# Kernel optimization log

Hardware: AMD Instinct MI355X
Metric: run time of the kernel (lower is better)

## Reference

```python
import jax, jax.numpy as jnp
import numpy as np

B, S, D, H = 4, 1024, 1024, 16
DH = D // H
RD = float(np.sqrt(D))


def linear_vdp(mu_a, var_a, mu_b, var_b):
    # Product of two independent random matrices: E[AB], Var[AB] (elementwise)
    mean = mu_a @ mu_b
    var = var_a @ var_b + var_a @ (mu_b ** 2) + (mu_a ** 2) @ var_b
    return mean, var


def softmax_vdp(a, var_a):
    # p = softmax(a); variance via squared Jacobian J_ij = p_i(delta_ij - p_j):
    # var_out_i = p_i^2 * (sum_j p_j^2 var_j + var_i * (1 - 2 p_i))
    p = jax.nn.softmax(a, axis=-1)
    s = jnp.sum(p * p * var_a, axis=-1, keepdims=True)
    var_out = p * p * (s + var_a * (1.0 - 2.0 * p))
    return p, var_out


def setup_inputs() -> dict:
    key = jax.random.key(0)
    ks = jax.random.split(key, 8)
    x = jax.random.normal(ks[0], (B, S, D), dtype=jnp.float32)
    var_x = jax.random.uniform(ks[1], (B, S, D), dtype=jnp.float32) * 0.1
    k = jax.random.normal(ks[2], (B, H, S, DH), dtype=jnp.float32)
    var_k = jax.random.uniform(ks[3], (B, H, S, DH), dtype=jnp.float32) * 0.1
    v = jax.random.normal(ks[4], (B, H, S, DH), dtype=jnp.float32)
    var_v = jax.random.uniform(ks[5], (B, H, S, DH), dtype=jnp.float32) * 0.1
    # LinearVDP(d, d, bias=False): weight mean + (positive) weight variance
    Wq_mu = jax.random.normal(ks[6], (D, D), dtype=jnp.float32) / np.sqrt(D)
    Wq_var = jax.random.uniform(ks[7], (D, D), dtype=jnp.float32) * (0.1 / D)
    return {"x": x, "var_x": var_x, "k": k, "var_k": var_k, "v": v,
            "var_v": var_v, "Wq_mu": Wq_mu, "Wq_var": Wq_var}


def reference(x, var_x, k, var_k, v, var_v, Wq_mu, Wq_var):
    # LinearVDP projection (y = x W^T with random weight)
    q = x @ Wq_mu.T
    var_q = var_x @ Wq_var.T + var_x @ (Wq_mu ** 2).T + (x ** 2) @ Wq_var.T
    # split heads: [B,S,D] -> [B,H,S,DH]
    q = q.reshape(B, S, H, DH).transpose(0, 2, 1, 3)
    var_q = var_q.reshape(B, S, H, DH).transpose(0, 2, 1, 3)
    # scores with variance propagation
    a, var_a = linear_vdp(q, var_q, jnp.swapaxes(k, 2, 3), jnp.swapaxes(var_k, 2, 3))
    a = a / RD
    var_a = var_a / (RD ** 2)
    # causal mask (-inf above diagonal) on the mean path only
    causal = jnp.triu(jnp.ones((S, S), dtype=bool), k=1)
    a = jnp.where(causal, -jnp.inf, a)
    a, var_a = softmax_vdp(a, var_a)
    # attention * values with variance propagation
    a, var_a = linear_vdp(a, var_a, v, var_v)
    # merge heads: [B,H,S,DH] -> [B,S,D]
    a = a.transpose(0, 2, 1, 3).reshape(B, S, D)
    var_a = var_a.transpose(0, 2, 1, 3).reshape(B, S, D)
    return x + a, var_a
```

## Files before the change

kernel.cpp:

```cpp
#include <hip/hip_runtime.h>
#include <hip/hip_bf16.h>
#include <math.h>

#define NB 4
#define NS 1024
#define ND 1024
#define NH 16
#define NDH 64
#define M4 4194304
#define M1 1048576

typedef float f16v __attribute__((ext_vector_type(16)));
typedef short bf8 __attribute__((ext_vector_type(8)));
typedef unsigned short ushort_t;

union U8 { bf8 v; unsigned u[4]; unsigned short s[8]; };

__device__ __forceinline__ unsigned pk(float lo, float hi) {
    __hip_bfloat162 h2 = __float22bfloat162_rn(make_float2(lo, hi));
    return *reinterpret_cast<unsigned*>(&h2);
}
__device__ __forceinline__ unsigned short f2b(float f) {
    unsigned u = __float_as_uint(f);
    unsigned r = (u + 0x7fffu + ((u >> 16) & 1u)) >> 16;
    return (unsigned short)r;
}
__device__ __forceinline__ float b2f(unsigned short h) {
    return __uint_as_float(((unsigned)h) << 16);
}
__device__ __forceinline__ f16v zero16() {
    f16v z;
    #pragma unroll
    for (int i = 0; i < 16; ++i) z[i] = 0.f;
    return z;
}
__device__ __forceinline__ void vscale(f16v& v, float s) {
    #pragma unroll
    for (int i = 0; i < 16; ++i) v[i] *= s;
}

__device__ __forceinline__ void gl_lds16(const ushort_t* g, ushort_t* l) {
    __builtin_amdgcn_global_load_lds(
        (const __attribute__((address_space(1))) unsigned int*)g,
        (__attribute__((address_space(3))) unsigned int*)l,
        16, 0, 0);
}

__device__ __forceinline__ bf8 mkB(unsigned p0, unsigned p1, unsigned p2, unsigned p3, int h) {
    unsigned own0 = h ? p2 : p0;
    unsigned own1 = h ? p3 : p1;
    unsigned ct0  = h ? p0 : p2;
    unsigned ct1  = h ? p1 : p3;
    unsigned x0 = (unsigned)__shfl_xor((int)ct0, 32);
    unsigned x1 = (unsigned)__shfl_xor((int)ct1, 32);
    U8 B;
    B.u[0] = h ? x0 : own0;
    B.u[1] = h ? x1 : own1;
    B.u[2] = h ? own0 : x0;
    B.u[3] = h ? own1 : x1;
    return B.v;
}


__global__ __launch_bounds__(256)
void prep_all(const float* __restrict__ x, const float* __restrict__ vx,
              const float* __restrict__ K,  const float* __restrict__ VK,
              const float* __restrict__ Vv, const float* __restrict__ VV,
              const float* __restrict__ Wm, const float* __restrict__ Wv,
              ushort_t* __restrict__ kmF, ushort_t* __restrict__ k2F, ushort_t* __restrict__ kvF,
              ushort_t* __restrict__ vmF, ushort_t* __restrict__ wF,  ushort_t* __restrict__ vvF,
              ushort_t* __restrict__ fx, ushort_t* __restrict__ fvx, ushort_t* __restrict__ fx2,
              ushort_t* __restrict__ fm, ushort_t* __restrict__ fw2, ushort_t* __restrict__ fv)
{
    __shared__ ushort_t Lm[2048], Lw[2048], Lv[2048];
    const int tid = threadIdx.x;
    const int bid = blockIdx.x;

    if (bid < 2048) {
        const int bh = bid >> 5, s = bid & 31;
        const int jp  = tid >> 3;
        const int dh0 = (tid & 7) * 8;
        const size_t gin = ((size_t)bh * NS + s * 32 + jp) * NDH + dh0;
        const size_t sbase = ((size_t)bh * 32 + s) * 2048;

        float kk[8], uu[8], vm[8], vv[8];
        *(float4*)(kk)   = *(const float4*)(K  + gin); *(float4*)(kk+4) = *(const float4*)(K  + gin + 4);
        *(float4*)(uu)   = *(const float4*)(VK + gin); *(float4*)(uu+4) = *(const float4*)(VK + gin + 4);
        *(float4*)(vm)   = *(const float4*)(Vv + gin); *(float4*)(vm+4) = *(const float4*)(Vv + gin + 4);
        *(float4*)(vv)   = *(const float4*)(VV + gin); *(float4*)(vv+4) = *(const float4*)(VV + gin + 4);

        const size_t kout = sbase + (size_t)((tid & 7) >> 1) * 512
                          + (jp + 32 * ((tid & 7) & 1)) * 8;
        unsigned o0[4], o1[4], o2[4];
        #pragma unroll
        for (int t = 0; t < 4; ++t) {
            o0[t] = pk(kk[2*t], kk[2*t+1]);
            o1[t] = pk(fmaf(kk[2*t],kk[2*t],uu[2*t]), fmaf(kk[2*t+1],kk[2*t+1],uu[2*t+1]));
            o2[t] = pk(uu[2*t], uu[2*t+1]);
        }
        *(uint4*)(kmF + kout) = make_uint4(o0[0],o0[1],o0[2],o0[3]);
        *(uint4*)(k2F + kout) = make_uint4(o1[0],o1[1],o1[2],o1[3]);
        *(uint4*)(kvF + kout) = make_uint4(o2[0],o2[1],o2[2],o2[3]);

        #pragma unroll
        for (int e = 0; e < 8; ++e) {
            const int dh = dh0 + e;
            const int idx = ((dh >> 5) * 2 + (jp >> 4)) * 512
                          + ((dh & 31) + 32 * ((jp >> 3) & 1)) * 8 + (jp & 7);
            Lm[idx] = f2b(vm[e]);
            Lw[idx] = f2b(fmaf(vm[e], vm[e], vv[e]));
            Lv[idx] = f2b(vv[e]);
        }
        __syncthreads();
        const size_t vout = sbase + (size_t)tid * 8;
        *(uint4*)(vmF + vout) = *(const uint4*)(Lm + tid * 8);
        *(uint4*)(wF  + vout) = *(const uint4*)(Lw + tid * 8);
        *(uint4*)(vvF + vout) = *(const uint4*)(Lv + tid * 8);
    } else {
        const size_t g = (size_t)(bid - 2048) * 256 + tid;
        if (g < 524288) {
            const size_t g0 = g * 8;
            const int row = (int)(g0 >> 10), k0 = (int)(g0 & 1023);
            const size_t fo = ((size_t)(row >> 5) * 64 + (k0 >> 4)) * 512
                            + ((row & 31) + 32 * ((k0 >> 3) & 1)) * 8;
            float a[8], c[8];
            *(float4*)(a)   = *(const float4*)(x + g0);  *(float4*)(a+4) = *(const float4*)(x + g0 + 4);
            *(float4*)(c)   = *(const float4*)(vx + g0); *(float4*)(c+4) = *(const float4*)(vx + g0 + 4);
            *(uint4*)(fx  + fo) = make_uint4(pk(a[0],a[1]), pk(a[2],a[3]), pk(a[4],a[5]), pk(a[6],a[7]));
            *(uint4*)(fvx + fo) = make_uint4(pk(c[0],c[1]), pk(c[2],c[3]), pk(c[4],c[5]), pk(c[6],c[7]));
            *(uint4*)(fx2 + fo) = make_uint4(pk(a[0]*a[0],a[1]*a[1]), pk(a[2]*a[2],a[3]*a[3]),
                                             pk(a[4]*a[4],a[5]*a[5]), pk(a[6]*a[6],a[7]*a[7]));
        } else {
            const size_t g0 = (g - 524288) * 8;
            const int row = (int)(g0 >> 10), k0 = (int)(g0 & 1023);
            const size_t fo = ((size_t)(row >> 5) * 64 + (k0 >> 4)) * 512
                            + ((row & 31) + 32 * ((k0 >> 3) & 1)) * 8;
            float a[8], c[8];
            *(float4*)(a)   = *(const float4*)(Wm + g0); *(float4*)(a+4) = *(const float4*)(Wm + g0 + 4);
            *(float4*)(c)   = *(const float4*)(Wv + g0); *(float4*)(c+4) = *(const float4*)(Wv + g0 + 4);
            *(uint4*)(fm  + fo) = make_uint4(pk(a[0],a[1]), pk(a[2],a[3]), pk(a[4],a[5]), pk(a[6],a[7]));
            *(uint4*)(fv  + fo) = make_uint4(pk(c[0],c[1]), pk(c[2],c[3]), pk(c[4],c[5]), pk(c[6],c[7]));
            *(uint4*)(fw2 + fo) = make_uint4(pk(fmaf(a[0],a[0],c[0]), fmaf(a[1],a[1],c[1])),
                                             pk(fmaf(a[2],a[2],c[2]), fmaf(a[3],a[3],c[3])),
                                             pk(fmaf(a[4],a[4],c[4]), fmaf(a[5],a[5],c[5])),
                                             pk(fmaf(a[6],a[6],c[6]), fmaf(a[7],a[7],c[7])));
        }
    }
}

__global__ __launch_bounds__(256, 2)
void qproj_b(const ushort_t* __restrict__ xplanes,
             const ushort_t* __restrict__ wplanes,
             ushort_t* __restrict__ qmF, ushort_t* __restrict__ vqF)
{
    __shared__ ushort_t wstg[3][12 * 512];

    const int tid  = threadIdx.x;
    const int w    = tid >> 6;
    const int lane = tid & 63;
    const int lh   = lane & 31;
    const int h    = lane >> 5;
    const int blk  = blockIdx.x;
    const int lb   = (blk & 7) * 64 + (blk >> 3);
    const int mb   = (lb >> 6) * 4 + ((lb & 63) >> 4);
    const int head = lb & 15;
    const int mt   = mb * 4 + w;
    const int nt   = head * 2 + (w & 1);

    f16v aQ0 = zero16(), aQ1 = zero16(), aV0 = zero16(), aV1 = zero16();

    const ushort_t* xb = xplanes + (size_t)mt * 64 * 512 + lane * 8;
    const ushort_t* wsrc = wplanes + ((size_t)nt * 64 + (w >> 1)) * 512 + lane * 8;

    #pragma unroll
    for (int q = 0; q < 3; ++q)
        gl_lds16(wsrc + (size_t)q * M1, &wstg[0][(3 * w + q) * 512 + lane * 8]);
    #pragma unroll
    for (int q = 0; q < 3; ++q)
        gl_lds16(wsrc + (size_t)q * M1 + 2 * 512, &wstg[1][(3 * w + q) * 512 + lane * 8]);

    bf8 xc[6], xn[6];
    #pragma unroll
    for (int kcL = 0; kcL < 2; ++kcL)
        #pragma unroll
        for (int q = 0; q < 3; ++q)
            xc[3 * kcL + q] = *(const bf8*)(xb + (size_t)q * M4 + kcL * 512);

    for (int t = 0; t < 32; ++t) {
        const int cur = t % 3;
        if (t < 31) asm volatile("s_waitcnt vmcnt(9)" ::: "memory");
        else        asm volatile("s_waitcnt vmcnt(6)" ::: "memory");
        __builtin_amdgcn_s_barrier();
        if (t + 2 < 32) {
            const int nxt = (t + 2) % 3;
            #pragma unroll
            for (int q = 0; q < 3; ++q)
                gl_lds16(wsrc + (size_t)q * M1 + (size_t)(2 * (t + 2)) * 512,
                         &wstg[nxt][(3 * w + q) * 512 + lane * 8]);
        }
        __builtin_amdgcn_sched_barrier(0);
        if (t + 1 < 32) {
            #pragma unroll
            for (int kcL = 0; kcL < 2; ++kcL)
                #pragma unroll
                for (int q = 0; q < 3; ++q)
                    xn[3 * kcL + q] = *(const bf8*)(xb + (size_t)q * M4 + (2 * (t + 1) + kcL) * 512);
        }
        const ushort_t* sc = wstg[cur];
        __builtin_amdgcn_s_setprio(1);
        #pragma unroll
        for (int kcL = 0; kcL < 2; ++kcL) {
            bf8 bx  = xc[3 * kcL + 0];
            bf8 bvx = xc[3 * kcL + 1];
            bf8 bx2 = xc[3 * kcL + 2];
            bf8 A0m = *(const bf8*)(sc + (3 * (2 * kcL + 0) + 0) * 512 + lane * 8);
            bf8 A0w = *(const bf8*)(sc + (3 * (2 * kcL + 0) + 1) * 512 + lane * 8);
            bf8 A0v = *(const bf8*)(sc + (3 * (2 * kcL + 0) + 2) * 512 + lane * 8);
            bf8 A1m = *(const bf8*)(sc + (3 * (2 * kcL + 1) + 0) * 512 + lane * 8);
            bf8 A1w = *(const bf8*)(sc + (3 * (2 * kcL + 1) + 1) * 512 + lane * 8);
            bf8 A1v = *(const bf8*)(sc + (3 * (2 * kcL + 1) + 2) * 512 + lane * 8);
            aQ0 = __builtin_amdgcn_mfma_f32_32x32x16_bf16(A0m, bx,  aQ0, 0, 0, 0);
            aV0 = __builtin_amdgcn_mfma_f32_32x32x16_bf16(A0w, bvx, aV0, 0, 0, 0);
            aV0 = __builtin_amdgcn_mfma_f32_32x32x16_bf16(A0v, bx2, aV0, 0, 0, 0);
            aQ1 = __builtin_amdgcn_mfma_f32_32x32x16_bf16(A1m, bx,  aQ1, 0, 0, 0);
            aV1 = __builtin_amdgcn_mfma_f32_32x32x16_bf16(A1w, bvx, aV1, 0, 0, 0);
            aV1 = __builtin_amdgcn_mfma_f32_32x32x16_bf16(A1v, bx2, aV1, 0, 0, 0);
        }
        __builtin_amdgcn_s_setprio(0);
        asm volatile("s_waitcnt lgkmcnt(0)" ::: "memory");
        __builtin_amdgcn_sched_barrier(0);
        #pragma unroll
        for (int q = 0; q < 6; ++q) xc[q] = xn[q];
    }

    const int mrow = mt * 32 + lh;
    const int b = mrow >> 10;
    const int rt = mt & 31;
    const size_t bh_base = ((size_t)(b * NH + head)) * 65536 + (size_t)rt * 2048;
    const float S1 = 0.03125f, S2 = 0.0009765625f;
    #pragma unroll
    for (int i = 0; i < 16; i += 2) {
        const int dh0 = (i & 3) + 8 * (i >> 2) + 4 * h;
        const size_t o = bh_base + (size_t)(dh0 >> 4) * 512
                       + (lh + 32 * ((dh0 >> 3) & 1)) * 8 + (dh0 & 7);
        *(unsigned*)(qmF + o)         = pk(aQ0[i]*S1, aQ0[i+1]*S1);
        *(unsigned*)(qmF + o + 1024)  = pk(aQ1[i]*S1, aQ1[i+1]*S1);
        *(unsigned*)(vqF + o)         = pk(aV0[i]*S2, aV0[i+1]*S2);
        *(unsigned*)(vqF + o + 1024)  = pk(aV1[i]*S2, aV1[i+1]*S2);
    }
}

__global__ __launch_bounds__(256, 2)
void attn_b(const ushort_t* __restrict__ qmF, const ushort_t* __restrict__ vqF,
            const ushort_t* __restrict__ planes,
            const float* __restrict__ x,
            float* __restrict__ out0, float* __restrict__ out1)
{
    __shared__ union {
        ushort_t stg[3][6 * 2048];
        float ep[128][66];
    } sm;

    const int tid  = threadIdx.x;
    const int w    = tid >> 6;
    const int lane = tid & 63;
    const int lh   = lane & 31;
    const int h    = lane >> 5;
    const int blk  = blockIdx.x;
    const int lb   = (blk & 7) * 64 + (blk >> 3);
    const int rb   = 7 - (lb & 7);
    const int bh   = lb >> 3;
    const int rt   = rb * 4 + w;
    const size_t base = (size_t)bh * 65536;

    bf8 fqm[4], fvq[4], fq2[4];
    {
        const ushort_t* qp = qmF + base + (size_t)rt * 2048 + lane * 8;
        const ushort_t* vp = vqF + base + (size_t)rt * 2048 + lane * 8;
        #pragma unroll
        for (int c = 0; c < 4; ++c) {
            fqm[c] = *(const bf8*)(qp + c * 512);
            fvq[c] = *(const bf8*)(vp + c * 512);
            U8 t; t.v = fqm[c];
            U8 r;
            #pragma unroll
            for (int k = 0; k < 4; ++k) {
                float q0 = b2f(t.s[2*k]), q1 = b2f(t.s[2*k+1]);
                r.u[k] = pk(q0*q0, q1*q1);
            }
            fq2[c] = r.v;
        }
    }

    f16v aN1[2], aN2w[2], aM2[2], aN3[2];
    #pragma unroll
    for (int dt = 0; dt < 2; ++dt) { aN1[dt]=zero16(); aN2w[dt]=zero16(); aM2[dt]=zero16(); aN3[dt]=zero16(); }
    float mrun = -INFINITY, Zrun = 0.f, S2run = 0.f;

    const int nstage = 4 * rb + 4;
    #pragma unroll
    for (int p = 0; p < 6; ++p)
        gl_lds16(planes + (size_t)p * M4 + base + w * 512 + lane * 8,
                 &sm.stg[0][p * 2048 + w * 512 + lane * 8]);
    #pragma unroll
    for (int p = 0; p < 6; ++p)
        gl_lds16(planes + (size_t)p * M4 + base + 2048 + w * 512 + lane * 8,
                 &sm.stg[1][p * 2048 + w * 512 + lane * 8]);

    for (int st = 0; st < nstage; ++st) {
        const int cur = st % 3;
        if (st + 2 < nstage) {
            const int nxt = (st + 2) % 3;
            #pragma unroll
            for (int p = 0; p < 6; ++p)
                gl_lds16(planes + (size_t)p * M4 + base + (size_t)(st + 2) * 2048 + w * 512 + lane * 8,
                         &sm.stg[nxt][p * 2048 + w * 512 + lane * 8]);
            asm volatile("s_waitcnt vmcnt(12)" ::: "memory");
        } else if (st + 1 < nstage) {
            asm volatile("s_waitcnt vmcnt(6)" ::: "memory");
        } else {
            asm volatile("s_waitcnt vmcnt(0)" ::: "memory");
        }
        __builtin_amdgcn_s_barrier();
        __builtin_amdgcn_sched_barrier(0);

        if (st <= rt) {
            __builtin_amdgcn_s_setprio(1);
            const ushort_t* sb = sm.stg[cur];
            f16v accA = zero16(), accU = zero16();
            #pragma unroll
            for (int c = 0; c < 4; ++c) {
                bf8 A0 = *(const bf8*)(sb + 0 * 2048 + c * 512 + lane * 8);
                bf8 A1 = *(const bf8*)(sb + 1 * 2048 + c * 512 + lane * 8);
                bf8 A2 = *(const bf8*)(sb + 2 * 2048 + c * 512 + lane * 8);
                accA = __builtin_amdgcn_mfma_f32_32x32x16_bf16(A0, fqm[c], accA, 0, 0, 0);
                accU = __builtin_amdgcn_mfma_f32_32x32x16_bf16(A1, fvq[c], accU, 0, 0, 0);
                accU = __builtin_amdgcn_mfma_f32_32x32x16_bf16(A2, fq2[c], accU, 0, 0, 0);
            }
            if (st == rt) {
                #pragma unroll
                for (int i = 0; i < 16; ++i) {
                    const int jl = (i & 3) + 8 * (i >> 2) + 4 * h;
                    if (jl > lh) accA[i] = -INFINITY;
                }
            }
            float t8[8];
            #pragma unroll
            for (int i = 0; i < 8; ++i) t8[i] = fmaxf(accA[i], accA[i + 8]);
            #pragma unroll
            for (int i = 0; i < 4; ++i) t8[i] = fmaxf(t8[i], t8[i + 4]);
            float mx = fmaxf(fmaxf(t8[0], t8[1]), fmaxf(t8[2], t8[3]));
            mx = fmaxf(mx, __shfl_xor(mx, 32));
            if (!__all(mx <= mrun + 8.f)) {
                const float mnew = fmaxf(mrun, mx);
                const float s1 = __expf(mrun - mnew);
                const float s2 = s1 * s1, s3 = s2 * s1;
                Zrun *= s1; S2run *= s2;
                #pragma unroll
                for (int dt = 0; dt < 2; ++dt) { vscale(aN1[dt],s1); vscale(aN2w[dt],s2); vscale(aM2[dt],s2); vscale(aN3[dt],s3); }
                mrun = mnew;
            }
            float zt[8], sq[8];
            #pragma unroll
            for (int i = 0; i < 16; ++i) accA[i] = __expf(accA[i] - mrun);
            #pragma unroll
            for (int i = 0; i < 8; ++i) {
                zt[i] = accA[i] + accA[i + 8];
                sq[i] = fmaf(accA[i] * accA[i], accU[i],
                             accA[i + 8] * accA[i + 8] * accU[i + 8]);
            }
            #pragma unroll
            for (int i = 0; i < 4; ++i) { zt[i] += zt[i + 4]; sq[i] += sq[i + 4]; }
            float Zt = (zt[0] + zt[1]) + (zt[2] + zt[3]);
            float St = (sq[0] + sq[1]) + (sq[2] + sq[3]);
            Zt += __shfl_xor(Zt, 32); St += __shfl_xor(St, 32);
            Zrun += Zt; S2run += St;

            #pragma unroll
            for (int c2 = 0; c2 < 2; ++c2) {
                unsigned pE[4], pE2[4], pEU[4], pE3[4];
                #pragma unroll
                for (int k = 0; k < 4; ++k) {
                    const int i0 = 8*c2 + 2*k;
                    const float e0 = accA[i0], e1 = accA[i0+1];
                    const float q0 = e0*e0, q1 = e1*e1;
                    const float t0 = q0*accU[i0], t1 = q1*accU[i0+1];
                    pE [k] = pk(e0, e1);
                    pE2[k] = pk(q0, q1);
                    pEU[k] = pk(t0, t1);
                    pE3[k] = pk(t0*e0, t1*e1);
                }
                bf8 BE  = mkB(pE [0], pE [1], pE [2], pE [3], h);
                bf8 BE2 = mkB(pE2[0], pE2[1], pE2[2], pE2[3], h);
                bf8 BEU = mkB(pEU[0], pEU[1], pEU[2], pEU[3], h);
                bf8 BE3 = mkB(pE3[0], pE3[1], pE3[2], pE3[3], h);
                #pragma unroll
                for (int dt = 0; dt < 2; ++dt) {
                    const ushort_t* vp = sb + 3 * 2048 + (dt * 2 + c2) * 512 + lane * 8;
                    bf8 Am = *(const bf8*)(vp + 0 * 2048);
                    bf8 Aw = *(const bf8*)(vp + 1 * 2048);
                    bf8 Av = *(const bf8*)(vp + 2 * 2048);
                    aN1[dt]  = __builtin_amdgcn_mfma_f32_32x32x16_bf16(Am, BE,  aN1[dt],  0, 0, 0);
                    aN2w[dt] = __builtin_amdgcn_mfma_f32_32x32x16_bf16(Aw, BE2, aN2w[dt], 0, 0, 0);
                    aM2[dt]  = __builtin_amdgcn_mfma_f32_32x32x16_bf16(Aw, BEU, aM2[dt],  0, 0, 0);
                    aM2[dt]  = __builtin_amdgcn_mfma_f32_32x32x16_bf16(Av, BE2, aM2[dt],  0, 0, 0);
                    aN3[dt]  = __builtin_amdgcn_mfma_f32_32x32x16_bf16(Aw, BE3, aN3[dt],  0, 0, 0);
                }
            }
            __builtin_amdgcn_s_setprio(0);
        }
        __builtin_amdgcn_sched_barrier(0);
        __builtin_amdgcn_s_barrier();
    }

    const float rZ  = 1.f / Zrun;
    const float rZ2 = rZ * rZ;
    const float sS  = S2run * rZ2;
    const int b = bh >> 4, head = bh & 15;

    #pragma unroll
    for (int dt = 0; dt < 2; ++dt)
        #pragma unroll
        for (int i = 0; i < 16; ++i) {
            const int col = 32*dt + (i & 3) + 8*(i >> 2) + 4*h;
            sm.ep[w*32 + lh][col] = aN1[dt][i] * rZ;
        }
    __syncthreads();
    {
        const int row = tid >> 1, half = (tid & 1) * 32;
        const size_t o = ((size_t)b * NS + rb*128 + row) * ND + head * NDH + half;
        #pragma unroll
        for (int q4 = 0; q4 < 32; q4 += 4) {
            float4 t = make_float4(sm.ep[row][half+q4], sm.ep[row][half+q4+1],
                                   sm.ep[row][half+q4+2], sm.ep[row][half+q4+3]);
            float4 xi = *(const float4*)(x + o + q4);
            *(float4*)(out0 + o + q4) = make_float4(t.x+xi.x, t.y+xi.y, t.z+xi.z, t.w+xi.w);
        }
    }
    __syncthreads();
    #pragma unroll
    for (int dt = 0; dt < 2; ++dt)
        #pragma unroll
        for (int i = 0; i < 16; ++i) {
            const int col = 32*dt + (i & 3) + 8*(i >> 2) + 4*h;
            sm.ep[w*32 + lh][col] = rZ2 * fmaf(sS, aN2w[dt][i], aM2[dt][i]) - 2.f*rZ2*rZ*aN3[dt][i];
        }
    __syncthreads();
    {
        const int row = tid >> 1, half = (tid & 1) * 32;
        const size_t o = ((size_t)b * NS + rb*128 + row) * ND + head * NDH + half;
        #pragma unroll
        for (int q4 = 0; q4 < 32; q4 += 4) {
            float4 t = make_float4(sm.ep[row][half+q4], sm.ep[row][half+q4+1],
                                   sm.ep[row][half+q4+2], sm.ep[row][half+q4+3]);
            *(float4*)(out1 + o + q4) = t;
        }
    }
}

extern "C" void kernel_launch(void* const* d_in, const int* in_sizes, int n_in,
                              void* d_out, int out_size, void* d_ws, size_t ws_size,
                              hipStream_t stream)
{
    (void)in_sizes; (void)n_in; (void)out_size; (void)ws_size;
    const float* x  = (const float*)d_in[0];
    const float* vx = (const float*)d_in[1];
    const float* K  = (const float*)d_in[2];
    const float* VK = (const float*)d_in[3];
    const float* Vv = (const float*)d_in[4];
    const float* VV = (const float*)d_in[5];
    const float* Wm = (const float*)d_in[6];
    const float* Wv = (const float*)d_in[7];

    float* out0 = (float*)d_out;
    float* out1 = out0 + (size_t)NB * NS * ND;

    ushort_t* qm  = (ushort_t*)d_ws;
    ushort_t* vq  = qm  + M4;
    ushort_t* kmF = vq  + M4;
    ushort_t* k2F = kmF + M4;
    ushort_t* kvF = k2F + M4;
    ushort_t* vmF = kvF + M4;
    ushort_t* wF  = vmF + M4;
    ushort_t* vvF = wF  + M4;
    ushort_t* fxF = vvF + M4;
    ushort_t* fvxF= fxF + M4;
    ushort_t* fx2F= fvxF+ M4;
    ushort_t* fmF = fx2F+ M4;
    ushort_t* fw2F= fmF + M1;
    ushort_t* fvF = fw2F+ M1;

    prep_all<<<4608, 256, 0, stream>>>(x, vx, K, VK, Vv, VV, Wm, Wv,
                                       kmF, k2F, kvF, vmF, wF, vvF,
                                       fxF, fvxF, fx2F, fmF, fw2F, fvF);
    qproj_b<<<512, 256, 0, stream>>>(fxF, fmF, qm, vq);
    attn_b<<<512, 256, 0, stream>>>(qm, vq, kmF, x, out0, out1);
}
```

Before: 167.9 us.

## Fuse Q projection into attention kernel, keeping Q fragments in registers

Merges the Q/var_q projection kernel into the attention kernel. Each block computes its own 128-row by head tile of q and var_q, packs the accumulators straight into MFMA operand fragments with mkB, and then runs attention. This drops the workspace round trip for qm/vq and one kernel launch. In exchange, the block-to-tile mapping changes so projection and attention tiles line up, which gives up the previous causal load-balancing order and may raise register pressure.

```diff
diff --git a/kernel.cpp b/kernel.cpp
--- a/kernel.cpp
+++ b/kernel.cpp
@@ -149,11 +149,17 @@
 }
 
 __global__ __launch_bounds__(256, 2)
-void qproj_b(const ushort_t* __restrict__ xplanes,
-             const ushort_t* __restrict__ wplanes,
-             ushort_t* __restrict__ qmF, ushort_t* __restrict__ vqF)
+void attn_fused(const ushort_t* __restrict__ xplanes,
+                const ushort_t* __restrict__ wplanes,
+                const ushort_t* __restrict__ planes,
+                const float* __restrict__ x,
+                float* __restrict__ out0, float* __restrict__ out1)
 {
-    __shared__ ushort_t wstg[3][12 * 512];
+    __shared__ union {
+        ushort_t wstg[3][12 * 512];
+        ushort_t stg[3][6 * 2048];
+        float ep[128][66];
+    } sm;
 
     const int tid  = threadIdx.x;
     const int w    = tid >> 6;
@@ -162,10 +168,17 @@
     const int h    = lane >> 5;
     const int blk  = blockIdx.x;
     const int lb   = (blk & 7) * 64 + (blk >> 3);
-    const int mb   = (lb >> 6) * 4 + ((lb & 63) >> 4);
+    const int xcd  = lb >> 6;
     const int head = lb & 15;
-    const int mt   = mb * 4 + w;
-    const int nt   = head * 2 + (w & 1);
+    const int g    = (lb >> 4) & 3;
+    const int b    = g;
+    const int rb   = (2 * g + xcd) & 7;
+    const int bh   = b * 16 + head;
+    const int rt   = rb * 4 + w;
+    const size_t base = (size_t)bh * 65536;
+
+    const int mt = b * 32 + rb * 4 + w;
+    const int nt = head * 2 + (w & 1);
 
     f16v aQ0 = zero16(), aQ1 = zero16(), aV0 = zero16(), aV1 = zero16();
 
@@ -174,10 +187,10 @@
 
     #pragma unroll
     for (int q = 0; q < 3; ++q)
-        gl_lds16(wsrc + (size_t)q * M1, &wstg[0][(3 * w + q) * 512 + lane * 8]);
+        gl_lds16(wsrc + (size_t)q * M1, &sm.wstg[0][(3 * w + q) * 512 + lane * 8]);
     #pragma unroll
     for (int q = 0; q < 3; ++q)
-        gl_lds16(wsrc + (size_t)q * M1 + 2 * 512, &wstg[1][(3 * w + q) * 512 + lane * 8]);
+        gl_lds16(wsrc + (size_t)q * M1 + 2 * 512, &sm.wstg[1][(3 * w + q) * 512 + lane * 8]);
 
     bf8 xc[6], xn[6];
     #pragma unroll
@@ -196,7 +209,7 @@
             #pragma unroll
             for (int q = 0; q < 3; ++q)
                 gl_lds16(wsrc + (size_t)q * M1 + (size_t)(2 * (t + 2)) * 512,
-                         &wstg[nxt][(3 * w + q) * 512 + lane * 8]);
+                         &sm.wstg[nxt][(3 * w + q) * 512 + lane * 8]);
         }
         __builtin_amdgcn_sched_barrier(0);
         if (t + 1 < 32) {
@@ -206,7 +219,7 @@
                 for (int q = 0; q < 3; ++q)
                     xn[3 * kcL + q] = *(const bf8*)(xb + (size_t)q * M4 + (2 * (t + 1) + kcL) * 512);
         }
-        const ushort_t* sc = wstg[cur];
+        const ushort_t* sc = sm.wstg[cur];
         __builtin_amdgcn_s_setprio(1);
         #pragma unroll
         for (int kcL = 0; kcL < 2; ++kcL) {
@@ -233,54 +246,21 @@
         for (int q = 0; q < 6; ++q) xc[q] = xn[q];
     }
 
-    const int mrow = mt * 32 + lh;
-    const int b = mrow >> 10;
-    const int rt = mt & 31;
-    const size_t bh_base = ((size_t)(b * NH + head)) * 65536 + (size_t)rt * 2048;
-    const float S1 = 0.03125f, S2 = 0.0009765625f;
-    #pragma unroll
-    for (int i = 0; i < 16; i += 2) {
-        const int dh0 = (i & 3) + 8 * (i >> 2) + 4 * h;
-        const size_t o = bh_base + (size_t)(dh0 >> 4) * 512
-                       + (lh + 32 * ((dh0 >> 3) & 1)) * 8 + (dh0 & 7);
-        *(unsigned*)(qmF + o)         = pk(aQ0[i]*S1, aQ0[i+1]*S1);
-        *(unsigned*)(qmF + o + 1024)  = pk(aQ1[i]*S1, aQ1[i+1]*S1);
-        *(unsigned*)(vqF + o)         = pk(aV0[i]*S2, aV0[i+1]*S2);
-        *(unsigned*)(vqF + o + 1024)  = pk(aV1[i]*S2, aV1[i+1]*S2);
-    }
-}
-
-__global__ __launch_bounds__(256, 2)
-void attn_b(const ushort_t* __restrict__ qmF, const ushort_t* __restrict__ vqF,
-            const ushort_t* __restrict__ planes,
-            const float* __restrict__ x,
-            float* __restrict__ out0, float* __restrict__ out1)
-{
-    __shared__ union {
-        ushort_t stg[3][6 * 2048];
-        float ep[128][66];
-    } sm;
-
-    const int tid  = threadIdx.x;
-    const int w    = tid >> 6;
-    const int lane = tid & 63;
-    const int lh   = lane & 31;
-    const int h    = lane >> 5;
-    const int blk  = blockIdx.x;
-    const int lb   = (blk & 7) * 64 + (blk >> 3);
-    const int rb   = 7 - (lb & 7);
-    const int bh   = lb >> 3;
-    const int rt   = rb * 4 + w;
-    const size_t base = (size_t)bh * 65536;
-
     bf8 fqm[4], fvq[4], fq2[4];
     {
-        const ushort_t* qp = qmF + base + (size_t)rt * 2048 + lane * 8;
-        const ushort_t* vp = vqF + base + (size_t)rt * 2048 + lane * 8;
+        const float S1 = 0.03125f, S2 = 0.0009765625f;
+        unsigned Uq[16], Uv[16];
+        #pragma unroll
+        for (int k = 0; k < 8; ++k) {
+            Uq[k]     = pk(aQ0[2*k] * S1, aQ0[2*k+1] * S1);
+            Uq[8 + k] = pk(aQ1[2*k] * S1, aQ1[2*k+1] * S1);
+            Uv[k]     = pk(aV0[2*k] * S2, aV0[2*k+1] * S2);
+            Uv[8 + k] = pk(aV1[2*k] * S2, aV1[2*k+1] * S2);
+        }
         #pragma unroll
         for (int c = 0; c < 4; ++c) {
-            fqm[c] = *(const bf8*)(qp + c * 512);
-            fvq[c] = *(const bf8*)(vp + c * 512);
+            fqm[c] = mkB(Uq[4*c], Uq[4*c+1], Uq[4*c+2], Uq[4*c+3], h);
+            fvq[c] = mkB(Uv[4*c], Uv[4*c+1], Uv[4*c+2], Uv[4*c+3], h);
             U8 t; t.v = fqm[c];
             U8 r;
             #pragma unroll
@@ -291,6 +271,9 @@
             fq2[c] = r.v;
         }
     }
+
+    asm volatile("s_waitcnt vmcnt(0) lgkmcnt(0)" ::: "memory");
+    __builtin_amdgcn_s_barrier();
 
     f16v aN1[2], aN2w[2], aM2[2], aN3[2];
     #pragma unroll
@@ -416,7 +399,6 @@
     const float rZ  = 1.f / Zrun;
     const float rZ2 = rZ * rZ;
     const float sS  = S2run * rZ2;
-    const int b = bh >> 4, head = bh & 15;
 
     #pragma unroll
     for (int dt = 0; dt < 2; ++dt)
@@ -475,9 +457,7 @@
     float* out0 = (float*)d_out;
     float* out1 = out0 + (size_t)NB * NS * ND;
 
-    ushort_t* qm  = (ushort_t*)d_ws;
-    ushort_t* vq  = qm  + M4;
-    ushort_t* kmF = vq  + M4;
+    ushort_t* kmF = (ushort_t*)d_ws;
     ushort_t* k2F = kmF + M4;
     ushort_t* kvF = k2F + M4;
     ushort_t* vmF = kvF + M4;
@@ -493,6 +473,5 @@
     prep_all<<<4608, 256, 0, stream>>>(x, vx, K, VK, Vv, VV, Wm, Wv,
                                        kmF, k2F, kvF, vmF, wF, vvF,
                                        fxF, fvxF, fx2F, fmF, fw2F, fvF);
-    qproj_b<<<512, 256, 0, stream>>>(fxF, fmF, qm, vq);
-    attn_b<<<512, 256, 0, stream>>>(qm, vq, kmF, x, out0, out1);
-}
+    attn_fused<<<512, 256, 0, stream>>>(fxF, fmF, kmF, x, out0, out1);
+}
```

Measured after the change: 154.9 us. 1.08x faster.
